# Kernel optimization log

Hardware: AMD Instinct MI355X
Metric: run time of the kernel (lower is better)

Reference implementation:

```python
import jax, jax.numpy as jnp
import numpy as np

B = 4096      # number of boards
H = 256       # n_hidden
SCALE = 0.0625  # 1/sqrt(H)
N_POLICY = 1858


def setup_inputs() -> dict:
    key = jax.random.key(0)
    ks = jax.random.split(key, 10)
    w_s = 1.0 / 16.0  # keep activations well-scaled
    return {
        "x": jax.random.normal(ks[0], (B * 64, H), jnp.float32),
        "w1": jax.random.normal(ks[1], (H, H), jnp.float32) * w_s,
        "b1": jax.random.normal(ks[2], (H,), jnp.float32) * w_s,
        "w2": jax.random.normal(ks[3], (H, H), jnp.float32) * w_s,
        "b2": jax.random.normal(ks[4], (H,), jnp.float32) * w_s,
        "w3": jax.random.normal(ks[5], (H, H), jnp.float32) * w_s,
        "b3": jax.random.normal(ks[6], (H,), jnp.float32) * w_s,
        "w4": jax.random.normal(ks[7], (4, H), jnp.float32) * w_s,
        "gather_idx": jax.random.randint(ks[8], (N_POLICY,), 0, 4288, jnp.int32),
    }


def reference(x, w1, b1, w2, b2, w3, b3, w4, gather_idx):
    out = jax.nn.relu(x @ w1.T + b1)                      # (B*64, H)
    q = (out @ w2.T + b2).reshape(-1, 64, H)              # (B, 64, H)
    k = (out @ w3.T + b3).reshape(-1, 64, H)              # (B, 64, H)
    logits = jnp.einsum("bqh,bkh->bqk", q, k) * SCALE     # (B, 64, 64)

    # promotion offsets from 8th-rank keys
    promo_keys = k[:, 56:64, :]                           # (B, 8, H)
    offs = jnp.einsum("bsh,ph->bps", promo_keys, w4)      # (B, 4, 8)
    offs = offs[:, :3, :] + offs[:, 3:4, :]               # (B, 3, 8) q/r/b + knight base
    off24 = jnp.transpose(offs, (0, 2, 1)).reshape(-1, 1, 24)  # (B,1,24) piece-fastest

    # knight promotion move logits: rank7 -> rank8 block
    n_promo = logits[:, 48:56, 56:64].reshape(-1, 64, 1)  # (B, 64, 1)
    n_promo = jnp.broadcast_to(n_promo, (n_promo.shape[0], 64, 3)).reshape(-1, 8, 24)

    promo = (off24 + n_promo).reshape(-1, 3, 64)          # (B, 3, 64)

    full = jnp.concatenate([logits, promo], axis=1).reshape(-1, 4288)  # (B, 4288)
    return jnp.take(full, gather_idx, axis=1)             # (B, 1858)
```

## Files before the change

kernel.cpp:

```cpp
#include <hip/hip_runtime.h>


typedef __bf16 bf16_t;
typedef __bf16 bf16x8 __attribute__((ext_vector_type(8)));
typedef float  f32x4  __attribute__((ext_vector_type(4)));

#define PSCALE 0.0625f
#define NPOL   1858
#define MFMA(a,b,c) __builtin_amdgcn_mfma_f32_16x16x32_bf16(a, b, c, 0, 0, 0)


__global__ void prep_w1(const float* __restrict__ w1, bf16_t* __restrict__ wfA) {
    int i = blockIdx.x * 256 + threadIdx.x;
    int j = i & 7, lane = (i >> 3) & 63, t = (i >> 9) & 7, n = (i >> 12) & 15;
    int row = n * 16 + (lane & 15);
    int col = t * 32 + (lane >> 4) * 8 + j;
    wfA[i] = (bf16_t)w1[row * 256 + col];
}

__global__ void prep_mat(const float* __restrict__ w2,
                         const float* __restrict__ w3,
                         bf16_t* __restrict__ wfM) {
    int m1 = blockIdx.x, m2 = threadIdx.x;
    float acc = 0.f;
    #pragma unroll 8
    for (int h = 0; h < 256; ++h)
        acc += w2[h * 256 + m1] * w3[h * 256 + m2];
    int t = m1 >> 5, quad = (m1 >> 3) & 3, j = m1 & 7;
    int n = m2 >> 4, l15 = m2 & 15;
    wfM[(((n * 8 + t) * 64) + (quad * 16 + l15)) * 8 + j] = (bf16_t)acc;
}

__global__ void prep_vecs(const float* __restrict__ w2,
                          const float* __restrict__ w3,
                          const float* __restrict__ b2,
                          const float* __restrict__ b3,
                          const float* __restrict__ w4,
                          float* __restrict__ flt) {
    int m = threadIdx.x;
    float c2 = 0.f, vv = 0.f, p0 = 0.f, p1 = 0.f, p2 = 0.f, p3 = 0.f;
    for (int h = 0; h < 256; ++h) {
        float w3h = w3[h * 256 + m];
        c2 += b2[h] * w3h;
        p0 += w4[h] * w3h;
        p1 += w4[256 + h] * w3h;
        p2 += w4[512 + h] * w3h;
        p3 += w4[768 + h] * w3h;
        vv += w2[h * 256 + m] * b3[h];
    }
    flt[m]        = c2;
    flt[256 + m]  = vv;
    flt[512 + m]  = p0;
    flt[768 + m]  = p1;
    flt[1024 + m] = p2;
    flt[1280 + m] = p3;
    if (m < 4) {
        float pb = 0.f;
        for (int h = 0; h < 256; ++h) pb += w4[m * 256 + h] * b3[h];
        flt[1536 + m] = pb;
    }
    if (m == 0) {
        float s = 0.f;
        for (int h = 0; h < 256; ++h) s += b2[h] * b3[h];
        flt[1540] = s;
    }
}


template <bool USE_WS>
__device__ __forceinline__ bf16x8 wfrag(const bf16_t* __restrict__ wl,
                                        const float* __restrict__ w,
                                        int n, int t, int lane) {
    if constexpr (USE_WS) {
        return *(const bf16x8*)(wl + (((n * 8 + t) * 64 + lane) << 3));
    } else {
        int l15 = lane & 15, quad = lane >> 4;
        const float* p = w + (n * 16 + l15) * 256 + t * 32 + quad * 8;
        f32x4 lo = *(const f32x4*)p;
        f32x4 hi = *(const f32x4*)(p + 4);
        bf16x8 v;
        v[0] = (bf16_t)lo[0]; v[1] = (bf16_t)lo[1];
        v[2] = (bf16_t)lo[2]; v[3] = (bf16_t)lo[3];
        v[4] = (bf16_t)hi[0]; v[5] = (bf16_t)hi[1];
        v[6] = (bf16_t)hi[2]; v[7] = (bf16_t)hi[3];
        return v;
    }
}

__device__ __forceinline__ int ks_off(int row, int col) {
    return ((row << 9) + (col << 1)) ^ ((row & 7) << 4);
}

__device__ __forceinline__ bf16x8 cvt8(const float* __restrict__ p) {
    f32x4 lo = *(const f32x4*)p;
    f32x4 hi = *(const f32x4*)(p + 4);
    bf16x8 v;
    v[0] = (bf16_t)lo[0]; v[1] = (bf16_t)lo[1];
    v[2] = (bf16_t)lo[2]; v[3] = (bf16_t)lo[3];
    v[4] = (bf16_t)hi[0]; v[5] = (bf16_t)hi[1];
    v[6] = (bf16_t)hi[2]; v[7] = (bf16_t)hi[3];
    return v;
}

__device__ __forceinline__ void mfma16(const bf16x8* inA, const bf16x8* inB,
                                       const bf16x8* w, f32x4& s0, f32x4& s1) {
    f32x4 a00 = {0.f,0.f,0.f,0.f}, a01 = {0.f,0.f,0.f,0.f};
    f32x4 a10 = {0.f,0.f,0.f,0.f}, a11 = {0.f,0.f,0.f,0.f};
    #pragma unroll
    for (int t = 0; t < 8; t += 2) {
        a00 = MFMA(inA[t],     w[t],     a00);
        a10 = MFMA(inB[t],     w[t],     a10);
        a01 = MFMA(inA[t + 1], w[t + 1], a01);
        a11 = MFMA(inB[t + 1], w[t + 1], a11);
    }
    s0 = a00 + a01;
    s1 = a10 + a11;
}

__device__ __forceinline__ void qtile_lds(const unsigned char* __restrict__ u_lds,
                                          const bf16x8* w, f32x4& s0, f32x4& s1,
                                          int quad, int l15, int R) {
    f32x4 a00 = {0.f,0.f,0.f,0.f}, a01 = {0.f,0.f,0.f,0.f};
    f32x4 a10 = {0.f,0.f,0.f,0.f}, a11 = {0.f,0.f,0.f,0.f};
    #pragma unroll
    for (int t = 0; t < 8; t += 2) {
        int oE = ks_off(R + l15, t * 32 + quad * 8);
        int oO = ks_off(R + l15, (t + 1) * 32 + quad * 8);
        bf16x8 xA0 = *(const bf16x8*)(u_lds + oE);
        bf16x8 xB0 = *(const bf16x8*)(u_lds + 32768 + oE);
        bf16x8 xA1 = *(const bf16x8*)(u_lds + oO);
        bf16x8 xB1 = *(const bf16x8*)(u_lds + 32768 + oO);
        a00 = MFMA(xA0, w[t],     a00);
        a10 = MFMA(xB0, w[t],     a10);
        a01 = MFMA(xA1, w[t + 1], a01);
        a11 = MFMA(xB1, w[t + 1], a11);
    }
    s0 = a00 + a01;
    s1 = a10 + a11;
}

template <bool RELU>
__device__ __forceinline__ void tile_store2(unsigned char* __restrict__ u_lds,
                                            const f32x4& sA, const f32x4& sB,
                                            float bv, int n,
                                            int quad, int l15, int R) {
    #pragma unroll
    for (int r2 = 0; r2 < 4; ++r2) {
        int off = ks_off(R + quad * 4 + r2, n * 16 + l15);
        float vA = sA[r2] + bv, vB = sB[r2] + bv;
        if (RELU) { vA = fmaxf(vA, 0.f); vB = fmaxf(vB, 0.f); }
        *(bf16_t*)(u_lds + off)         = (bf16_t)vA;
        *(bf16_t*)(u_lds + 32768 + off) = (bf16_t)vB;
    }
}

template <bool USE_WS, bool RELU>
__device__ __forceinline__ void layer2b(const bf16x8* inA, const bf16x8* inB,
                                        const bf16_t* __restrict__ wl,
                                        const float* __restrict__ wraw,
                                        const float* __restrict__ bias,
                                        unsigned char* __restrict__ u_lds,
                                        int lane, int quad, int l15, int R) {
    bf16x8 wA[4], wB[4];
    #pragma unroll
    for (int t = 0; t < 4; ++t)
        wA[t] = wfrag<USE_WS>(wl, wraw, 0, t, lane);

    #pragma unroll
    for (int n = 0; n < 16; ++n) {
        #pragma unroll
        for (int t = 0; t < 4; ++t)
            wB[t] = wfrag<USE_WS>(wl, wraw, n, 4 + t, lane);

        f32x4 aA0 = {0.f,0.f,0.f,0.f}, aA1 = {0.f,0.f,0.f,0.f};
        f32x4 aB0 = {0.f,0.f,0.f,0.f}, aB1 = {0.f,0.f,0.f,0.f};
        aA0 = MFMA(inA[0], wA[0], aA0);  aB0 = MFMA(inB[0], wA[0], aB0);
        aA1 = MFMA(inA[1], wA[1], aA1);  aB1 = MFMA(inB[1], wA[1], aB1);
        aA0 = MFMA(inA[2], wA[2], aA0);  aB0 = MFMA(inB[2], wA[2], aB0);
        aA1 = MFMA(inA[3], wA[3], aA1);  aB1 = MFMA(inB[3], wA[3], aB1);

        if (n < 15) {
            #pragma unroll
            for (int t = 0; t < 4; ++t)
                wA[t] = wfrag<USE_WS>(wl, wraw, n + 1, t, lane);
        }

        aA0 = MFMA(inA[4], wB[0], aA0);  aB0 = MFMA(inB[4], wB[0], aB0);
        aA1 = MFMA(inA[5], wB[1], aA1);  aB1 = MFMA(inB[5], wB[1], aB1);
        aA0 = MFMA(inA[6], wB[2], aA0);  aB0 = MFMA(inB[6], wB[2], aB0);
        aA1 = MFMA(inA[7], wB[3], aA1);  aB1 = MFMA(inB[7], wB[3], aB1);

        tile_store2<RELU>(u_lds, aA0 + aA1, aB0 + aB1,
                          bias[n * 16 + l15], n, quad, l15, R);
    }
}

__global__ __launch_bounds__(256, 2)
void policy_fused(const float* __restrict__ x,
                  const bf16_t* __restrict__ wfA,
                  const bf16_t* __restrict__ wfM,
                  const float* __restrict__ flt,
                  const float* __restrict__ b1,
                  const int*   __restrict__ gidx,
                  float* __restrict__ out,
                  int nbat) {
    __shared__ __align__(16) unsigned char u_lds[2 * 32768];
    __shared__ __align__(16) bf16_t qscr[4][2][16 * 40];
    __shared__ float promoLDS[2][4][8];
    __shared__ float patchLDS[2][8][8];
    __shared__ float qbLDS[2][64];

    const int tid  = threadIdx.x;
    const int lane = tid & 63;
    const int wv   = tid >> 6;
    const int quad = lane >> 4;
    const int l15  = lane & 15;
    const int R    = wv * 16;

    const int bat0 = blockIdx.x * 2;
    const bool has1 = (bat0 + 1) < nbat;
    const int bat1 = has1 ? bat0 + 1 : bat0;

    bf16x8 xaA[8], xaB[8];
    {
        const float* xr0 = x + ((size_t)bat0 * 64 + R + l15) * 256;
        const float* xr1 = x + ((size_t)bat1 * 64 + R + l15) * 256;
        #pragma unroll
        for (int t = 0; t < 8; ++t) {
            xaA[t] = cvt8(xr0 + t * 32 + quad * 8);
            xaB[t] = cvt8(xr1 + t * 32 + quad * 8);
        }
    }

    layer2b<true, true>(xaA, xaB, wfA, nullptr, b1, u_lds, lane, quad, l15, R);

    {
        float qbA = flt[1540], qbB = qbA;
        const float* vvec = flt + 256;
        #pragma unroll
        for (int t = 0; t < 8; ++t) {
            int off = ks_off(R + l15, t * 32 + quad * 8);
            bf16x8 oA = *(const bf16x8*)(u_lds + off);
            bf16x8 oB = *(const bf16x8*)(u_lds + 32768 + off);
            f32x4 va = *(const f32x4*)(vvec + t * 32 + quad * 8);
            f32x4 vb = *(const f32x4*)(vvec + t * 32 + quad * 8 + 4);
            qbA += (float)oA[0]*va[0] + (float)oA[1]*va[1]
                 + (float)oA[2]*va[2] + (float)oA[3]*va[3]
                 + (float)oA[4]*vb[0] + (float)oA[5]*vb[1]
                 + (float)oA[6]*vb[2] + (float)oA[7]*vb[3];
            qbB += (float)oB[0]*va[0] + (float)oB[1]*va[1]
                 + (float)oB[2]*va[2] + (float)oB[3]*va[3]
                 + (float)oB[4]*vb[0] + (float)oB[5]*vb[1]
                 + (float)oB[6]*vb[2] + (float)oB[7]*vb[3];
        }
        qbA += __shfl_xor(qbA, 16);  qbA += __shfl_xor(qbA, 32);
        qbB += __shfl_xor(qbB, 16);  qbB += __shfl_xor(qbB, 32);
        if (lane < 16) {
            qbLDS[0][R + lane] = qbA;
            qbLDS[1][R + lane] = qbB;
        }
    }

    bf16x8 wc[8], wn[8];
    #pragma unroll
    for (int t = 0; t < 8; ++t)
        wc[t] = wfrag<true>(wfM, nullptr, 0, t, lane);

    __syncthreads();

    f32x4 laA[4], laB[4];
    #pragma unroll
    for (int n = 0; n < 4; ++n) {
        laA[n] = (f32x4){0.f,0.f,0.f,0.f};
        laB[n] = (f32x4){0.f,0.f,0.f,0.f};
    }
    {
        bf16_t* qsA = &qscr[wv][0][0];
        bf16_t* qsB = &qscr[wv][1][0];

        #pragma unroll
        for (int t8 = 0; t8 < 8; ++t8) {
            const int n0 = 2 * t8, n1 = n0 + 1;

            #pragma unroll
            for (int t = 0; t < 8; ++t)
                wn[t] = wfrag<true>(wfM, nullptr, n1, t, lane);
            {
                f32x4 sA, sB;
                qtile_lds(u_lds, wc, sA, sB, quad, l15, R);
                float bv = flt[n0 * 16 + l15];
                #pragma unroll
                for (int r2 = 0; r2 < 4; ++r2) {
                    int qo = (quad * 4 + r2) * 40 + l15;
                    qsA[qo] = (bf16_t)(sA[r2] + bv);
                    qsB[qo] = (bf16_t)(sB[r2] + bv);
                }
            }

            if (t8 < 7) {
                #pragma unroll
                for (int t = 0; t < 8; ++t)
                    wc[t] = wfrag<true>(wfM, nullptr, n0 + 2, t, lane);
            }
            {
                f32x4 sA, sB;
                qtile_lds(u_lds, wn, sA, sB, quad, l15, R);
                float bv = flt[n1 * 16 + l15];
                #pragma unroll
                for (int r2 = 0; r2 < 4; ++r2) {
                    int qo = (quad * 4 + r2) * 40 + 16 + l15;
                    qsA[qo] = (bf16_t)(sA[r2] + bv);
                    qsB[qo] = (bf16_t)(sB[r2] + bv);
                }
            }

            bf16x8 qaA = *(const bf16x8*)(qsA + l15 * 40 + quad * 8);
            bf16x8 qaB = *(const bf16x8*)(qsB + l15 * 40 + quad * 8);
            #pragma unroll
            for (int np = 0; np < 4; ++np) {
                int ko = ks_off(np * 16 + l15, t8 * 32 + quad * 8);
                bf16x8 kA = *(const bf16x8*)(u_lds + ko);
                bf16x8 kB = *(const bf16x8*)(u_lds + 32768 + ko);
                laA[np] = MFMA(qaA, kA, laA[np]);
                laB[np] = MFMA(qaB, kB, laB[np]);
            }
        }
    }

    float qbra[4], qbrb[4];
    #pragma unroll
    for (int r2 = 0; r2 < 4; ++r2) {
        qbra[r2] = qbLDS[0][R + quad * 4 + r2];
        qbrb[r2] = qbLDS[1][R + quad * 4 + r2];
    }

    {
        int s = lane >> 3, seg = lane & 7;
        const float* wrow = flt + 512 + wv * 256;
        #pragma unroll
        for (int b = 0; b < 2; ++b) {
            const unsigned char* kb = u_lds + b * 32768;
            float p = 0.f;
            #pragma unroll
            for (int m = 0; m < 4; ++m) {
                bf16x8 kv = *(const bf16x8*)(kb + ks_off(56 + s, seg * 32 + m * 8));
                f32x4 wa = *(const f32x4*)(wrow + seg * 32 + m * 8);
                f32x4 wb = *(const f32x4*)(wrow + seg * 32 + m * 8 + 4);
                p += (float)kv[0] * wa[0] + (float)kv[1] * wa[1]
                   + (float)kv[2] * wa[2] + (float)kv[3] * wa[3]
                   + (float)kv[4] * wb[0] + (float)kv[5] * wb[1]
                   + (float)kv[6] * wb[2] + (float)kv[7] * wb[3];
            }
            p += __shfl_down(p, 4);
            p += __shfl_down(p, 2);
            p += __shfl_down(p, 1);
            if (seg == 0) promoLDS[b][wv][s] = p + flt[1536 + wv];
        }
    }

    if (wv == 3 && quad < 2 && l15 >= 8) {
        #pragma unroll
        for (int r2 = 0; r2 < 4; ++r2) {
            patchLDS[0][quad * 4 + r2][l15 - 8] = (laA[3][r2] + qbra[r2]) * PSCALE;
            patchLDS[1][quad * 4 + r2][l15 - 8] = (laB[3][r2] + qbrb[r2]) * PSCALE;
        }
    }

    __syncthreads();

    float* fb0 = (float*)u_lds;
    float* fb1 = (float*)(u_lds + 32768);
    #pragma unroll
    for (int n = 0; n < 4; ++n) {
        #pragma unroll
        for (int r2 = 0; r2 < 4; ++r2) {
            int idx = (R + quad * 4 + r2) * 64 + n * 16 + l15;
            fb0[idx] = (laA[n][r2] + qbra[r2]) * PSCALE;
            fb1[idx] = (laB[n][r2] + qbrb[r2]) * PSCALE;
        }
    }

    if (tid < 192) {
        int u = tid >> 6, vv2 = tid & 63;
        int mm = u * 64 + vv2;
        int r_ = mm / 24, c_ = mm - r_ * 24;
        int c3 = c_ / 3, cp = c_ - c3 * 3;
        fb0[(64 + u) * 64 + vv2] =
            promoLDS[0][cp][c3] + promoLDS[0][3][c3] + patchLDS[0][r_][c3];
        fb1[(64 + u) * 64 + vv2] =
            promoLDS[1][cp][c3] + promoLDS[1][3][c3] + patchLDS[1][r_][c3];
    }

    __syncthreads();

    {
        float* orow0 = out + (size_t)bat0 * NPOL;
        float* orow1 = out + (size_t)(bat0 + 1) * NPOL;
        int   idxv[8];
        float v0[8], v1[8];
        #pragma unroll
        for (int i = 0; i < 8; ++i) {
            int g = tid + i * 256;
            idxv[i] = (g < NPOL) ? gidx[g] : 0;
        }
        #pragma unroll
        for (int i = 0; i < 8; ++i) {
            v0[i] = fb0[idxv[i]];
            v1[i] = fb1[idxv[i]];
        }
        #pragma unroll
        for (int i = 0; i < 8; ++i) {
            int g = tid + i * 256;
            if (g < NPOL) {
                orow0[g] = v0[i];
                if (has1) orow1[g] = v1[i];
            }
        }
    }
}

__global__ __launch_bounds__(256, 2)
void policy_main(const float* __restrict__ x,
                 const float* __restrict__ w1,
                 const float* __restrict__ w2,
                 const float* __restrict__ w3,
                 const float* __restrict__ b1,
                 const float* __restrict__ b2,
                 const float* __restrict__ b3,
                 const float* __restrict__ w4,
                 const int*   __restrict__ gidx,
                 float* __restrict__ out,
                 int nbat) {
    __shared__ __align__(16) unsigned char u_lds[2 * 32768];
    __shared__ __align__(16) bf16_t qscr[4][2][16 * 40];
    __shared__ float promoLDS[2][4][8];
    __shared__ float patchLDS[2][8][8];

    const int tid  = threadIdx.x;
    const int lane = tid & 63;
    const int wv   = tid >> 6;
    const int quad = lane >> 4;
    const int l15  = lane & 15;
    const int R    = wv * 16;

    const int bat0 = blockIdx.x * 2;
    const bool has1 = (bat0 + 1) < nbat;
    const int bat1 = has1 ? bat0 + 1 : bat0;

    bf16x8 xaA[8], xaB[8];
    {
        const float* xr0 = x + ((size_t)bat0 * 64 + R + l15) * 256;
        const float* xr1 = x + ((size_t)bat1 * 64 + R + l15) * 256;
        #pragma unroll
        for (int t = 0; t < 8; ++t) {
            xaA[t] = cvt8(xr0 + t * 32 + quad * 8);
            xaB[t] = cvt8(xr1 + t * 32 + quad * 8);
        }
    }

    layer2b<false, true>(xaA, xaB, nullptr, w1, b1, u_lds, lane, quad, l15, R);
    bf16x8 oaA[8], oaB[8];
    #pragma unroll
    for (int t = 0; t < 8; ++t) {
        int off = ks_off(R + l15, t * 32 + quad * 8);
        oaA[t] = *(const bf16x8*)(u_lds + off);
        oaB[t] = *(const bf16x8*)(u_lds + 32768 + off);
    }

    layer2b<false, false>(oaA, oaB, nullptr, w3, b3, u_lds, lane, quad, l15, R);

    __syncthreads();

    f32x4 laA[4], laB[4];
    #pragma unroll
    for (int n = 0; n < 4; ++n) {
        laA[n] = (f32x4){0.f,0.f,0.f,0.f};
        laB[n] = (f32x4){0.f,0.f,0.f,0.f};
    }
    {
        bf16_t* qsA = &qscr[wv][0][0];
        bf16_t* qsB = &qscr[wv][1][0];
        bf16x8 wA[4], wB[4];
        #pragma unroll
        for (int t = 0; t < 4; ++t)
            wA[t] = wfrag<false>(nullptr, w2, 0, t, lane);

        #pragma unroll
        for (int t8 = 0; t8 < 8; ++t8) {
            const int n0 = 2 * t8, n1 = n0 + 1;
            #pragma unroll
            for (int t = 0; t < 4; ++t)
                wB[t] = wfrag<false>(nullptr, w2, n0, 4 + t, lane);
            {
                f32x4 cA0 = {0.f,0.f,0.f,0.f}, cA1 = {0.f,0.f,0.f,0.f};
                f32x4 cB0 = {0.f,0.f,0.f,0.f}, cB1 = {0.f,0.f,0.f,0.f};
                cA0 = MFMA(oaA[0], wA[0], cA0);  cB0 = MFMA(oaB[0], wA[0], cB0);
                cA1 = MFMA(oaA[1], wA[1], cA1);  cB1 = MFMA(oaB[1], wA[1], cB1);
                cA0 = MFMA(oaA[2], wA[2], cA0);  cB0 = MFMA(oaB[2], wA[2], cB0);
                cA1 = MFMA(oaA[3], wA[3], cA1);  cB1 = MFMA(oaB[3], wA[3], cB1);
                #pragma unroll
                for (int t = 0; t < 4; ++t)
                    wA[t] = wfrag<false>(nullptr, w2, n1, t, lane);
                cA0 = MFMA(oaA[4], wB[0], cA0);  cB0 = MFMA(oaB[4], wB[0], cB0);
                cA1 = MFMA(oaA[5], wB[1], cA1);  cB1 = MFMA(oaB[5], wB[1], cB1);
                cA0 = MFMA(oaA[6], wB[2], cA0);  cB0 = MFMA(oaB[6], wB[2], cB0);
                cA1 = MFMA(oaA[7], wB[3], cA1);  cB1 = MFMA(oaB[7], wB[3], cB1);
                f32x4 sA = cA0 + cA1, sB = cB0 + cB1;
                float bv = b2[n0 * 16 + l15];
                #pragma unroll
                for (int r2 = 0; r2 < 4; ++r2) {
                    int qo = (quad * 4 + r2) * 40 + l15;
                    qsA[qo] = (bf16_t)(sA[r2] + bv);
                    qsB[qo] = (bf16_t)(sB[r2] + bv);
                }
            }
            #pragma unroll
            for (int t = 0; t < 4; ++t)
                wB[t] = wfrag<false>(nullptr, w2, n1, 4 + t, lane);
            {
                f32x4 cA0 = {0.f,0.f,0.f,0.f}, cA1 = {0.f,0.f,0.f,0.f};
                f32x4 cB0 = {0.f,0.f,0.f,0.f}, cB1 = {0.f,0.f,0.f,0.f};
                cA0 = MFMA(oaA[0], wA[0], cA0);  cB0 = MFMA(oaB[0], wA[0], cB0);
                cA1 = MFMA(oaA[1], wA[1], cA1);  cB1 = MFMA(oaB[1], wA[1], cB1);
                cA0 = MFMA(oaA[2], wA[2], cA0);  cB0 = MFMA(oaB[2], wA[2], cB0);
                cA1 = MFMA(oaA[3], wA[3], cA1);  cB1 = MFMA(oaB[3], wA[3], cB1);
                if (t8 < 7) {
                    #pragma unroll
                    for (int t = 0; t < 4; ++t)
                        wA[t] = wfrag<false>(nullptr, w2, n0 + 2, t, lane);
                }
                cA0 = MFMA(oaA[4], wB[0], cA0);  cB0 = MFMA(oaB[4], wB[0], cB0);
                cA1 = MFMA(oaA[5], wB[1], cA1);  cB1 = MFMA(oaB[5], wB[1], cB1);
                cA0 = MFMA(oaA[6], wB[2], cA0);  cB0 = MFMA(oaB[6], wB[2], cB0);
                cA1 = MFMA(oaA[7], wB[3], cA1);  cB1 = MFMA(oaB[7], wB[3], cB1);
                f32x4 sA = cA0 + cA1, sB = cB0 + cB1;
                float bv = b2[n1 * 16 + l15];
                #pragma unroll
                for (int r2 = 0; r2 < 4; ++r2) {
                    int qo = (quad * 4 + r2) * 40 + 16 + l15;
                    qsA[qo] = (bf16_t)(sA[r2] + bv);
                    qsB[qo] = (bf16_t)(sB[r2] + bv);
                }
            }
            bf16x8 qaA = *(const bf16x8*)(qsA + l15 * 40 + quad * 8);
            bf16x8 qaB = *(const bf16x8*)(qsB + l15 * 40 + quad * 8);
            #pragma unroll
            for (int np = 0; np < 4; ++np) {
                int ko = ks_off(np * 16 + l15, t8 * 32 + quad * 8);
                bf16x8 kA = *(const bf16x8*)(u_lds + ko);
                bf16x8 kB = *(const bf16x8*)(u_lds + 32768 + ko);
                laA[np] = MFMA(qaA, kA, laA[np]);
                laB[np] = MFMA(qaB, kB, laB[np]);
            }
        }
    }

    {
        int s = lane >> 3, seg = lane & 7;
        const float* wrow = w4 + wv * 256;
        #pragma unroll
        for (int b = 0; b < 2; ++b) {
            const unsigned char* kb = u_lds + b * 32768;
            float p = 0.f;
            #pragma unroll
            for (int m = 0; m < 4; ++m) {
                bf16x8 kv = *(const bf16x8*)(kb + ks_off(56 + s, seg * 32 + m * 8));
                f32x4 wa = *(const f32x4*)(wrow + seg * 32 + m * 8);
                f32x4 wb = *(const f32x4*)(wrow + seg * 32 + m * 8 + 4);
                p += (float)kv[0] * wa[0] + (float)kv[1] * wa[1]
                   + (float)kv[2] * wa[2] + (float)kv[3] * wa[3]
                   + (float)kv[4] * wb[0] + (float)kv[5] * wb[1]
                   + (float)kv[6] * wb[2] + (float)kv[7] * wb[3];
            }
            p += __shfl_down(p, 4);
            p += __shfl_down(p, 2);
            p += __shfl_down(p, 1);
            if (seg == 0) promoLDS[b][wv][s] = p;
        }
    }

    if (wv == 3 && quad < 2 && l15 >= 8) {
        #pragma unroll
        for (int r2 = 0; r2 < 4; ++r2) {
            patchLDS[0][quad * 4 + r2][l15 - 8] = laA[3][r2] * PSCALE;
            patchLDS[1][quad * 4 + r2][l15 - 8] = laB[3][r2] * PSCALE;
        }
    }

    __syncthreads();

    float* fb0 = (float*)u_lds;
    float* fb1 = (float*)(u_lds + 32768);
    #pragma unroll
    for (int n = 0; n < 4; ++n) {
        #pragma unroll
        for (int r2 = 0; r2 < 4; ++r2) {
            int idx = (R + quad * 4 + r2) * 64 + n * 16 + l15;
            fb0[idx] = laA[n][r2] * PSCALE;
            fb1[idx] = laB[n][r2] * PSCALE;
        }
    }

    if (tid < 192) {
        int u = tid >> 6, vv2 = tid & 63;
        int mm = u * 64 + vv2;
        int r_ = mm / 24, c_ = mm - r_ * 24;
        int c3 = c_ / 3, cp = c_ - c3 * 3;
        fb0[(64 + u) * 64 + vv2] =
            promoLDS[0][cp][c3] + promoLDS[0][3][c3] + patchLDS[0][r_][c3];
        fb1[(64 + u) * 64 + vv2] =
            promoLDS[1][cp][c3] + promoLDS[1][3][c3] + patchLDS[1][r_][c3];
    }

    __syncthreads();

    {
        float* orow0 = out + (size_t)bat0 * NPOL;
        float* orow1 = out + (size_t)(bat0 + 1) * NPOL;
        int   idxv[8];
        float v0[8], v1[8];
        #pragma unroll
        for (int i = 0; i < 8; ++i) {
            int g = tid + i * 256;
            idxv[i] = (g < NPOL) ? gidx[g] : 0;
        }
        #pragma unroll
        for (int i = 0; i < 8; ++i) {
            v0[i] = fb0[idxv[i]];
            v1[i] = fb1[idxv[i]];
        }
        #pragma unroll
        for (int i = 0; i < 8; ++i) {
            int g = tid + i * 256;
            if (g < NPOL) {
                orow0[g] = v0[i];
                if (has1) orow1[g] = v1[i];
            }
        }
    }
}

extern "C" void kernel_launch(void* const* d_in, const int* in_sizes, int n_in,
                              void* d_out, int out_size, void* d_ws, size_t ws_size,
                              hipStream_t stream) {
    const float* x    = (const float*)d_in[0];
    const float* w1   = (const float*)d_in[1];
    const float* b1   = (const float*)d_in[2];
    const float* w2   = (const float*)d_in[3];
    const float* b2   = (const float*)d_in[4];
    const float* w3   = (const float*)d_in[5];
    const float* b3   = (const float*)d_in[6];
    const float* w4   = (const float*)d_in[7];
    const int*   gidx = (const int*)d_in[8];
    float* out = (float*)d_out;

    int nbat = in_sizes[0] / (64 * 256);
    int nblk = (nbat + 1) / 2;
    const size_t ws_needed = 262144 + 8192;

    if (ws_size >= ws_needed) {
        bf16_t* wfA = (bf16_t*)d_ws;
        bf16_t* wfM = wfA + 65536;
        float*  flt = (float*)((char*)d_ws + 262144);
        prep_w1  <<<256, 256, 0, stream>>>(w1, wfA);
        prep_mat <<<256, 256, 0, stream>>>(w2, w3, wfM);
        prep_vecs<<<1,   256, 0, stream>>>(w2, w3, b2, b3, w4, flt);
        policy_fused<<<nblk, 256, 0, stream>>>(
            x, wfA, wfM, flt, b1, gidx, out, nbat);
    } else {
        policy_main<<<nblk, 256, 0, stream>>>(
            x, w1, w2, w3, b1, b2, b3, w4, gidx, out, nbat);
    }
}
```

Measured before the change: 523.9 us.

## Split fused policy kernel across 8 waves with half-column layers

Replaces the 256-thread fused kernel with a 512-thread version. Each pair of waves now shares a 16-row group, and each wave computes half of the output columns of layer 1 and of the folded q·M layer. The q-projection is materialised in a second 64KB LDS buffer, so the per-tile q scratch and the fused q-tile/logit loop go away; logits are then computed per wave over its half of the key columns. The goal is more waves to hide MFMA and LDS latency and no redundant weight-fragment loads per wave. In exchange the block uses about 128KB of LDS, which may cap occupancy at one block per CU despite the launch bounds, and it adds barriers. The fallback kernel is also refactored to use shared helpers.

Result: slower. 536.1 us (+2.3%).

```diff
diff --git a/kernel.cpp b/kernel.cpp
--- a/kernel.cpp
+++ b/kernel.cpp
@@ -102,75 +102,24 @@
     return v;
 }
 
-__device__ __forceinline__ void mfma16(const bf16x8* inA, const bf16x8* inB,
-                                       const bf16x8* w, f32x4& s0, f32x4& s1) {
-    f32x4 a00 = {0.f,0.f,0.f,0.f}, a01 = {0.f,0.f,0.f,0.f};
-    f32x4 a10 = {0.f,0.f,0.f,0.f}, a11 = {0.f,0.f,0.f,0.f};
-    #pragma unroll
-    for (int t = 0; t < 8; t += 2) {
-        a00 = MFMA(inA[t],     w[t],     a00);
-        a10 = MFMA(inB[t],     w[t],     a10);
-        a01 = MFMA(inA[t + 1], w[t + 1], a01);
-        a11 = MFMA(inB[t + 1], w[t + 1], a11);
-    }
-    s0 = a00 + a01;
-    s1 = a10 + a11;
-}
-
-__device__ __forceinline__ void qtile_lds(const unsigned char* __restrict__ u_lds,
-                                          const bf16x8* w, f32x4& s0, f32x4& s1,
-                                          int quad, int l15, int R) {
-    f32x4 a00 = {0.f,0.f,0.f,0.f}, a01 = {0.f,0.f,0.f,0.f};
-    f32x4 a10 = {0.f,0.f,0.f,0.f}, a11 = {0.f,0.f,0.f,0.f};
-    #pragma unroll
-    for (int t = 0; t < 8; t += 2) {
-        int oE = ks_off(R + l15, t * 32 + quad * 8);
-        int oO = ks_off(R + l15, (t + 1) * 32 + quad * 8);
-        bf16x8 xA0 = *(const bf16x8*)(u_lds + oE);
-        bf16x8 xB0 = *(const bf16x8*)(u_lds + 32768 + oE);
-        bf16x8 xA1 = *(const bf16x8*)(u_lds + oO);
-        bf16x8 xB1 = *(const bf16x8*)(u_lds + 32768 + oO);
-        a00 = MFMA(xA0, w[t],     a00);
-        a10 = MFMA(xB0, w[t],     a10);
-        a01 = MFMA(xA1, w[t + 1], a01);
-        a11 = MFMA(xB1, w[t + 1], a11);
-    }
-    s0 = a00 + a01;
-    s1 = a10 + a11;
-}
-
 template <bool RELU>
-__device__ __forceinline__ void tile_store2(unsigned char* __restrict__ u_lds,
-                                            const f32x4& sA, const f32x4& sB,
-                                            float bv, int n,
+__device__ __forceinline__ void layer_half8(const bf16x8* inA, const bf16x8* inB,
+                                            const bf16_t* __restrict__ wl,
+                                            const float* __restrict__ bias,
+                                            unsigned char* __restrict__ dst,
+                                            int nb, int lane,
                                             int quad, int l15, int R) {
-    #pragma unroll
-    for (int r2 = 0; r2 < 4; ++r2) {
-        int off = ks_off(R + quad * 4 + r2, n * 16 + l15);
-        float vA = sA[r2] + bv, vB = sB[r2] + bv;
-        if (RELU) { vA = fmaxf(vA, 0.f); vB = fmaxf(vB, 0.f); }
-        *(bf16_t*)(u_lds + off)         = (bf16_t)vA;
-        *(bf16_t*)(u_lds + 32768 + off) = (bf16_t)vB;
-    }
-}
-
-template <bool USE_WS, bool RELU>
-__device__ __forceinline__ void layer2b(const bf16x8* inA, const bf16x8* inB,
-                                        const bf16_t* __restrict__ wl,
-                                        const float* __restrict__ wraw,
-                                        const float* __restrict__ bias,
-                                        unsigned char* __restrict__ u_lds,
-                                        int lane, int quad, int l15, int R) {
     bf16x8 wA[4], wB[4];
     #pragma unroll
     for (int t = 0; t < 4; ++t)
-        wA[t] = wfrag<USE_WS>(wl, wraw, 0, t, lane);
-
-    #pragma unroll
-    for (int n = 0; n < 16; ++n) {
+        wA[t] = wfrag<true>(wl, nullptr, nb, t, lane);
+
+    #pragma unroll
+    for (int k = 0; k < 8; ++k) {
+        const int n = nb + k;
         #pragma unroll
         for (int t = 0; t < 4; ++t)
-            wB[t] = wfrag<USE_WS>(wl, wraw, n, 4 + t, lane);
+            wB[t] = wfrag<true>(wl, nullptr, n, 4 + t, lane);
 
         f32x4 aA0 = {0.f,0.f,0.f,0.f}, aA1 = {0.f,0.f,0.f,0.f};
         f32x4 aB0 = {0.f,0.f,0.f,0.f}, aB1 = {0.f,0.f,0.f,0.f};
@@ -179,10 +128,10 @@
         aA0 = MFMA(inA[2], wA[2], aA0);  aB0 = MFMA(inB[2], wA[2], aB0);
         aA1 = MFMA(inA[3], wA[3], aA1);  aB1 = MFMA(inB[3], wA[3], aB1);
 
-        if (n < 15) {
+        if (k < 7) {
             #pragma unroll
             for (int t = 0; t < 4; ++t)
-                wA[t] = wfrag<USE_WS>(wl, wraw, n + 1, t, lane);
+                wA[t] = wfrag<true>(wl, nullptr, n + 1, t, lane);
         }
 
         aA0 = MFMA(inA[4], wB[0], aA0);  aB0 = MFMA(inB[4], wB[0], aB0);
@@ -190,22 +139,30 @@
         aA0 = MFMA(inA[6], wB[2], aA0);  aB0 = MFMA(inB[6], wB[2], aB0);
         aA1 = MFMA(inA[7], wB[3], aA1);  aB1 = MFMA(inB[7], wB[3], aB1);
 
-        tile_store2<RELU>(u_lds, aA0 + aA1, aB0 + aB1,
-                          bias[n * 16 + l15], n, quad, l15, R);
-    }
-}
-
-__global__ __launch_bounds__(256, 2)
-void policy_fused(const float* __restrict__ x,
-                  const bf16_t* __restrict__ wfA,
-                  const bf16_t* __restrict__ wfM,
-                  const float* __restrict__ flt,
-                  const float* __restrict__ b1,
-                  const int*   __restrict__ gidx,
-                  float* __restrict__ out,
-                  int nbat) {
-    __shared__ __align__(16) unsigned char u_lds[2 * 32768];
-    __shared__ __align__(16) bf16_t qscr[4][2][16 * 40];
+        f32x4 sA = aA0 + aA1, sB = aB0 + aB1;
+        float bv = bias[n * 16 + l15];
+        #pragma unroll
+        for (int r2 = 0; r2 < 4; ++r2) {
+            int off = ks_off(R + quad * 4 + r2, n * 16 + l15);
+            float vA = sA[r2] + bv, vB = sB[r2] + bv;
+            if (RELU) { vA = fmaxf(vA, 0.f); vB = fmaxf(vB, 0.f); }
+            *(bf16_t*)(dst + off)         = (bf16_t)vA;
+            *(bf16_t*)(dst + 32768 + off) = (bf16_t)vB;
+        }
+    }
+}
+
+__global__ __launch_bounds__(512, 2)
+void policy_fused8(const float* __restrict__ x,
+                   const bf16_t* __restrict__ wfA,
+                   const bf16_t* __restrict__ wfM,
+                   const float* __restrict__ flt,
+                   const float* __restrict__ b1,
+                   const int*   __restrict__ gidx,
+                   float* __restrict__ out,
+                   int nbat) {
+    __shared__ __align__(16) unsigned char u_lds[65536];
+    __shared__ __align__(16) unsigned char q2b[65536];
     __shared__ float promoLDS[2][4][8];
     __shared__ float patchLDS[2][8][8];
     __shared__ float qbLDS[2][64];
@@ -213,9 +170,12 @@
     const int tid  = threadIdx.x;
     const int lane = tid & 63;
     const int wv   = tid >> 6;
+    const int rg   = wv >> 1;
+    const int ch   = wv & 1;
     const int quad = lane >> 4;
     const int l15  = lane & 15;
-    const int R    = wv * 16;
+    const int R    = rg * 16;
+    const int NB   = ch * 8;
 
     const int bat0 = blockIdx.x * 2;
     const bool has1 = (bat0 + 1) < nbat;
@@ -232,137 +192,92 @@
         }
     }
 
-    layer2b<true, true>(xaA, xaB, wfA, nullptr, b1, u_lds, lane, quad, l15, R);
-
-    {
-        float qbA = flt[1540], qbB = qbA;
+    layer_half8<true>(xaA, xaB, wfA, b1, u_lds, NB, lane, quad, l15, R);
+
+    __syncthreads();
+
+    bf16x8 oaA[8], oaB[8];
+    #pragma unroll
+    for (int t = 0; t < 8; ++t) {
+        int off = ks_off(R + l15, t * 32 + quad * 8);
+        oaA[t] = *(const bf16x8*)(u_lds + off);
+        oaB[t] = *(const bf16x8*)(u_lds + 32768 + off);
+    }
+
+    layer_half8<false>(oaA, oaB, wfM, flt, q2b, NB, lane, quad, l15, R);
+
+    {
+        const bf16x8* oc = ch ? oaB : oaA;
+        float qb = flt[1540];
         const float* vvec = flt + 256;
         #pragma unroll
         for (int t = 0; t < 8; ++t) {
-            int off = ks_off(R + l15, t * 32 + quad * 8);
-            bf16x8 oA = *(const bf16x8*)(u_lds + off);
-            bf16x8 oB = *(const bf16x8*)(u_lds + 32768 + off);
             f32x4 va = *(const f32x4*)(vvec + t * 32 + quad * 8);
             f32x4 vb = *(const f32x4*)(vvec + t * 32 + quad * 8 + 4);
-            qbA += (float)oA[0]*va[0] + (float)oA[1]*va[1]
-                 + (float)oA[2]*va[2] + (float)oA[3]*va[3]
-                 + (float)oA[4]*vb[0] + (float)oA[5]*vb[1]
-                 + (float)oA[6]*vb[2] + (float)oA[7]*vb[3];
-            qbB += (float)oB[0]*va[0] + (float)oB[1]*va[1]
-                 + (float)oB[2]*va[2] + (float)oB[3]*va[3]
-                 + (float)oB[4]*vb[0] + (float)oB[5]*vb[1]
-                 + (float)oB[6]*vb[2] + (float)oB[7]*vb[3];
-        }
-        qbA += __shfl_xor(qbA, 16);  qbA += __shfl_xor(qbA, 32);
-        qbB += __shfl_xor(qbB, 16);  qbB += __shfl_xor(qbB, 32);
-        if (lane < 16) {
-            qbLDS[0][R + lane] = qbA;
-            qbLDS[1][R + lane] = qbB;
-        }
-    }
-
-    bf16x8 wc[8], wn[8];
-    #pragma unroll
-    for (int t = 0; t < 8; ++t)
-        wc[t] = wfrag<true>(wfM, nullptr, 0, t, lane);
+            qb += (float)oc[t][0]*va[0] + (float)oc[t][1]*va[1]
+                + (float)oc[t][2]*va[2] + (float)oc[t][3]*va[3]
+                + (float)oc[t][4]*vb[0] + (float)oc[t][5]*vb[1]
+                + (float)oc[t][6]*vb[2] + (float)oc[t][7]*vb[3];
+        }
+        qb += __shfl_xor(qb, 16);
+        qb += __shfl_xor(qb, 32);
+        if (lane < 16) qbLDS[ch][R + lane] = qb;
+    }
 
     __syncthreads();
 
-    f32x4 laA[4], laB[4];
-    #pragma unroll
-    for (int n = 0; n < 4; ++n) {
-        laA[n] = (f32x4){0.f,0.f,0.f,0.f};
-        laB[n] = (f32x4){0.f,0.f,0.f,0.f};
-    }
-    {
-        bf16_t* qsA = &qscr[wv][0][0];
-        bf16_t* qsB = &qscr[wv][1][0];
-
-        #pragma unroll
-        for (int t8 = 0; t8 < 8; ++t8) {
-            const int n0 = 2 * t8, n1 = n0 + 1;
-
-            #pragma unroll
-            for (int t = 0; t < 8; ++t)
-                wn[t] = wfrag<true>(wfM, nullptr, n1, t, lane);
-            {
-                f32x4 sA, sB;
-                qtile_lds(u_lds, wc, sA, sB, quad, l15, R);
-                float bv = flt[n0 * 16 + l15];
-                #pragma unroll
-                for (int r2 = 0; r2 < 4; ++r2) {
-                    int qo = (quad * 4 + r2) * 40 + l15;
-                    qsA[qo] = (bf16_t)(sA[r2] + bv);
-                    qsB[qo] = (bf16_t)(sB[r2] + bv);
-                }
-            }
-
-            if (t8 < 7) {
-                #pragma unroll
-                for (int t = 0; t < 8; ++t)
-                    wc[t] = wfrag<true>(wfM, nullptr, n0 + 2, t, lane);
-            }
-            {
-                f32x4 sA, sB;
-                qtile_lds(u_lds, wn, sA, sB, quad, l15, R);
-                float bv = flt[n1 * 16 + l15];
-                #pragma unroll
-                for (int r2 = 0; r2 < 4; ++r2) {
-                    int qo = (quad * 4 + r2) * 40 + 16 + l15;
-                    qsA[qo] = (bf16_t)(sA[r2] + bv);
-                    qsB[qo] = (bf16_t)(sB[r2] + bv);
-                }
-            }
-
-            bf16x8 qaA = *(const bf16x8*)(qsA + l15 * 40 + quad * 8);
-            bf16x8 qaB = *(const bf16x8*)(qsB + l15 * 40 + quad * 8);
-            #pragma unroll
-            for (int np = 0; np < 4; ++np) {
-                int ko = ks_off(np * 16 + l15, t8 * 32 + quad * 8);
-                bf16x8 kA = *(const bf16x8*)(u_lds + ko);
-                bf16x8 kB = *(const bf16x8*)(u_lds + 32768 + ko);
-                laA[np] = MFMA(qaA, kA, laA[np]);
-                laB[np] = MFMA(qaB, kB, laB[np]);
-            }
-        }
-    }
-
-    float qbra[4], qbrb[4];
-    #pragma unroll
-    for (int r2 = 0; r2 < 4; ++r2) {
-        qbra[r2] = qbLDS[0][R + quad * 4 + r2];
-        qbrb[r2] = qbLDS[1][R + quad * 4 + r2];
+    bf16x8 qaA[8], qaB[8];
+    #pragma unroll
+    for (int t = 0; t < 8; ++t) {
+        int off = ks_off(R + l15, t * 32 + quad * 8);
+        qaA[t] = *(const bf16x8*)(q2b + off);
+        qaB[t] = *(const bf16x8*)(q2b + 32768 + off);
+    }
+
+    f32x4 laA[2], laB[2];
+    laA[0] = (f32x4){0.f,0.f,0.f,0.f}; laA[1] = (f32x4){0.f,0.f,0.f,0.f};
+    laB[0] = (f32x4){0.f,0.f,0.f,0.f}; laB[1] = (f32x4){0.f,0.f,0.f,0.f};
+    #pragma unroll
+    for (int t8 = 0; t8 < 8; ++t8) {
+        #pragma unroll
+        for (int npl = 0; npl < 2; ++npl) {
+            int ko = ks_off((2 * ch + npl) * 16 + l15, t8 * 32 + quad * 8);
+            bf16x8 kA = *(const bf16x8*)(u_lds + ko);
+            bf16x8 kB = *(const bf16x8*)(u_lds + 32768 + ko);
+            laA[npl] = MFMA(qaA[t8], kA, laA[npl]);
+            laB[npl] = MFMA(qaB[t8], kB, laB[npl]);
+        }
     }
 
     {
         int s = lane >> 3, seg = lane & 7;
-        const float* wrow = flt + 512 + wv * 256;
-        #pragma unroll
-        for (int b = 0; b < 2; ++b) {
-            const unsigned char* kb = u_lds + b * 32768;
-            float p = 0.f;
-            #pragma unroll
-            for (int m = 0; m < 4; ++m) {
-                bf16x8 kv = *(const bf16x8*)(kb + ks_off(56 + s, seg * 32 + m * 8));
-                f32x4 wa = *(const f32x4*)(wrow + seg * 32 + m * 8);
-                f32x4 wb = *(const f32x4*)(wrow + seg * 32 + m * 8 + 4);
-                p += (float)kv[0] * wa[0] + (float)kv[1] * wa[1]
-                   + (float)kv[2] * wa[2] + (float)kv[3] * wa[3]
-                   + (float)kv[4] * wb[0] + (float)kv[5] * wb[1]
-                   + (float)kv[6] * wb[2] + (float)kv[7] * wb[3];
-            }
-            p += __shfl_down(p, 4);
-            p += __shfl_down(p, 2);
-            p += __shfl_down(p, 1);
-            if (seg == 0) promoLDS[b][wv][s] = p + flt[1536 + wv];
-        }
-    }
-
-    if (wv == 3 && quad < 2 && l15 >= 8) {
+        const float* wrow = flt + 512 + rg * 256;
+        const unsigned char* kb = u_lds + ch * 32768;
+        float pacc = 0.f;
+        #pragma unroll
+        for (int m = 0; m < 4; ++m) {
+            bf16x8 kv = *(const bf16x8*)(kb + ks_off(56 + s, seg * 32 + m * 8));
+            f32x4 wa = *(const f32x4*)(wrow + seg * 32 + m * 8);
+            f32x4 wb = *(const f32x4*)(wrow + seg * 32 + m * 8 + 4);
+            pacc += (float)kv[0] * wa[0] + (float)kv[1] * wa[1]
+                  + (float)kv[2] * wa[2] + (float)kv[3] * wa[3]
+                  + (float)kv[4] * wb[0] + (float)kv[5] * wb[1]
+                  + (float)kv[6] * wb[2] + (float)kv[7] * wb[3];
+        }
+        pacc += __shfl_down(pacc, 4);
+        pacc += __shfl_down(pacc, 2);
+        pacc += __shfl_down(pacc, 1);
+        if (seg == 0) promoLDS[ch][rg][s] = pacc + flt[1536 + rg];
+    }
+
+    if (wv == 7 && quad < 2 && l15 >= 8) {
         #pragma unroll
         for (int r2 = 0; r2 < 4; ++r2) {
-            patchLDS[0][quad * 4 + r2][l15 - 8] = (laA[3][r2] + qbra[r2]) * PSCALE;
-            patchLDS[1][quad * 4 + r2][l15 - 8] = (laB[3][r2] + qbrb[r2]) * PSCALE;
+            int row = 48 + quad * 4 + r2;
+            patchLDS[0][quad * 4 + r2][l15 - 8] =
+                (laA[1][r2] + qbLDS[0][row]) * PSCALE;
+            patchLDS[1][quad * 4 + r2][l15 - 8] =
+                (laB[1][r2] + qbLDS[1][row]) * PSCALE;
         }
     }
 
@@ -370,25 +285,34 @@
 
     float* fb0 = (float*)u_lds;
     float* fb1 = (float*)(u_lds + 32768);
-    #pragma unroll
-    for (int n = 0; n < 4; ++n) {
+    {
+        float qb0[4], qb1[4];
         #pragma unroll
         for (int r2 = 0; r2 < 4; ++r2) {
-            int idx = (R + quad * 4 + r2) * 64 + n * 16 + l15;
-            fb0[idx] = (laA[n][r2] + qbra[r2]) * PSCALE;
-            fb1[idx] = (laB[n][r2] + qbrb[r2]) * PSCALE;
-        }
-    }
-
-    if (tid < 192) {
-        int u = tid >> 6, vv2 = tid & 63;
+            qb0[r2] = qbLDS[0][R + quad * 4 + r2];
+            qb1[r2] = qbLDS[1][R + quad * 4 + r2];
+        }
+        #pragma unroll
+        for (int npl = 0; npl < 2; ++npl) {
+            #pragma unroll
+            for (int r2 = 0; r2 < 4; ++r2) {
+                int idx = (R + quad * 4 + r2) * 64 + (2 * ch + npl) * 16 + l15;
+                fb0[idx] = (laA[npl][r2] + qb0[r2]) * PSCALE;
+                fb1[idx] = (laB[npl][r2] + qb1[r2]) * PSCALE;
+            }
+        }
+    }
+
+    if (tid < 384) {
+        int b  = tid / 192;
+        int m  = tid - b * 192;
+        int u  = m >> 6, vv2 = m & 63;
         int mm = u * 64 + vv2;
         int r_ = mm / 24, c_ = mm - r_ * 24;
         int c3 = c_ / 3, cp = c_ - c3 * 3;
-        fb0[(64 + u) * 64 + vv2] =
-            promoLDS[0][cp][c3] + promoLDS[0][3][c3] + patchLDS[0][r_][c3];
-        fb1[(64 + u) * 64 + vv2] =
-            promoLDS[1][cp][c3] + promoLDS[1][3][c3] + patchLDS[1][r_][c3];
+        float* fb = b ? fb1 : fb0;
+        fb[(64 + u) * 64 + vv2] =
+            promoLDS[b][cp][c3] + promoLDS[b][3][c3] + patchLDS[b][r_][c3];
     }
 
     __syncthreads();
@@ -396,25 +320,83 @@
     {
         float* orow0 = out + (size_t)bat0 * NPOL;
         float* orow1 = out + (size_t)(bat0 + 1) * NPOL;
-        int   idxv[8];
-        float v0[8], v1[8];
-        #pragma unroll
-        for (int i = 0; i < 8; ++i) {
-            int g = tid + i * 256;
+        int   idxv[4];
+        float v0[4], v1[4];
+        #pragma unroll
+        for (int i = 0; i < 4; ++i) {
+            int g = tid + i * 512;
             idxv[i] = (g < NPOL) ? gidx[g] : 0;
         }
         #pragma unroll
-        for (int i = 0; i < 8; ++i) {
+        for (int i = 0; i < 4; ++i) {
             v0[i] = fb0[idxv[i]];
             v1[i] = fb1[idxv[i]];
         }
         #pragma unroll
-        for (int i = 0; i < 8; ++i) {
-            int g = tid + i * 256;
+        for (int i = 0; i < 4; ++i) {
+            int g = tid + i * 512;
             if (g < NPOL) {
                 orow0[g] = v0[i];
                 if (has1) orow1[g] = v1[i];
             }
+        }
+    }
+}
+
+__device__ __forceinline__ void mfma16f(const bf16x8* inA, const bf16x8* inB,
+                                        const bf16x8* w, f32x4& s0, f32x4& s1) {
+    f32x4 a00 = {0.f,0.f,0.f,0.f}, a01 = {0.f,0.f,0.f,0.f};
+    f32x4 a10 = {0.f,0.f,0.f,0.f}, a11 = {0.f,0.f,0.f,0.f};
+    #pragma unroll
+    for (int t = 0; t < 8; t += 2) {
+        a00 = MFMA(inA[t],     w[t],     a00);
+        a10 = MFMA(inB[t],     w[t],     a10);
+        a01 = MFMA(inA[t + 1], w[t + 1], a01);
+        a11 = MFMA(inB[t + 1], w[t + 1], a11);
+    }
+    s0 = a00 + a01;
+    s1 = a10 + a11;
+}
+
+template <bool RELU>
+__device__ __forceinline__ void layer_raw(const bf16x8* inA, const bf16x8* inB,
+                                          const float* __restrict__ wraw,
+                                          const float* __restrict__ bias,
+                                          unsigned char* __restrict__ u_lds,
+                                          int lane, int quad, int l15, int R) {
+    bf16x8 wA[4], wB[4];
+    #pragma unroll
+    for (int t = 0; t < 4; ++t)
+        wA[t] = wfrag<false>(nullptr, wraw, 0, t, lane);
+    #pragma unroll
+    for (int n = 0; n < 16; ++n) {
+        #pragma unroll
+        for (int t = 0; t < 4; ++t)
+            wB[t] = wfrag<false>(nullptr, wraw, n, 4 + t, lane);
+        f32x4 aA0 = {0.f,0.f,0.f,0.f}, aA1 = {0.f,0.f,0.f,0.f};
+        f32x4 aB0 = {0.f,0.f,0.f,0.f}, aB1 = {0.f,0.f,0.f,0.f};
+        aA0 = MFMA(inA[0], wA[0], aA0);  aB0 = MFMA(inB[0], wA[0], aB0);
+        aA1 = MFMA(inA[1], wA[1], aA1);  aB1 = MFMA(inB[1], wA[1], aB1);
+        aA0 = MFMA(inA[2], wA[2], aA0);  aB0 = MFMA(inB[2], wA[2], aB0);
+        aA1 = MFMA(inA[3], wA[3], aA1);  aB1 = MFMA(inB[3], wA[3], aB1);
+        if (n < 15) {
+            #pragma unroll
+            for (int t = 0; t < 4; ++t)
+                wA[t] = wfrag<false>(nullptr, wraw, n + 1, t, lane);
+        }
+        aA0 = MFMA(inA[4], wB[0], aA0);  aB0 = MFMA(inB[4], wB[0], aB0);
+        aA1 = MFMA(inA[5], wB[1], aA1);  aB1 = MFMA(inB[5], wB[1], aB1);
+        aA0 = MFMA(inA[6], wB[2], aA0);  aB0 = MFMA(inB[6], wB[2], aB0);
+        aA1 = MFMA(inA[7], wB[3], aA1);  aB1 = MFMA(inB[7], wB[3], aB1);
+        f32x4 sA = aA0 + aA1, sB = aB0 + aB1;
+        float bv = bias[n * 16 + l15];
+        #pragma unroll
+        for (int r2 = 0; r2 < 4; ++r2) {
+            int off = ks_off(R + quad * 4 + r2, n * 16 + l15);
+            float vA = sA[r2] + bv, vB = sB[r2] + bv;
+            if (RELU) { vA = fmaxf(vA, 0.f); vB = fmaxf(vB, 0.f); }
+            *(bf16_t*)(u_lds + off)         = (bf16_t)vA;
+            *(bf16_t*)(u_lds + 32768 + off) = (bf16_t)vB;
         }
     }
 }
@@ -458,7 +440,7 @@
         }
     }
 
-    layer2b<false, true>(xaA, xaB, nullptr, w1, b1, u_lds, lane, quad, l15, R);
+    layer_raw<true>(xaA, xaB, w1, b1, u_lds, lane, quad, l15, R);
     bf16x8 oaA[8], oaB[8];
     #pragma unroll
     for (int t = 0; t < 8; ++t) {
@@ -467,7 +449,7 @@
         oaB[t] = *(const bf16x8*)(u_lds + 32768 + off);
     }
 
-    layer2b<false, false>(oaA, oaB, nullptr, w3, b3, u_lds, lane, quad, l15, R);
+    layer_raw<false>(oaA, oaB, w3, b3, u_lds, lane, quad, l15, R);
 
     __syncthreads();
 
@@ -492,20 +474,10 @@
             for (int t = 0; t < 4; ++t)
                 wB[t] = wfrag<false>(nullptr, w2, n0, 4 + t, lane);
             {
-                f32x4 cA0 = {0.f,0.f,0.f,0.f}, cA1 = {0.f,0.f,0.f,0.f};
-                f32x4 cB0 = {0.f,0.f,0.f,0.f}, cB1 = {0.f,0.f,0.f,0.f};
-                cA0 = MFMA(oaA[0], wA[0], cA0);  cB0 = MFMA(oaB[0], wA[0], cB0);
-                cA1 = MFMA(oaA[1], wA[1], cA1);  cB1 = MFMA(oaB[1], wA[1], cB1);
-                cA0 = MFMA(oaA[2], wA[2], cA0);  cB0 = MFMA(oaB[2], wA[2], cB0);
-                cA1 = MFMA(oaA[3], wA[3], cA1);  cB1 = MFMA(oaB[3], wA[3], cB1);
-                #pragma unroll
-                for (int t = 0; t < 4; ++t)
-                    wA[t] = wfrag<false>(nullptr, w2, n1, t, lane);
-                cA0 = MFMA(oaA[4], wB[0], cA0);  cB0 = MFMA(oaB[4], wB[0], cB0);
-                cA1 = MFMA(oaA[5], wB[1], cA1);  cB1 = MFMA(oaB[5], wB[1], cB1);
-                cA0 = MFMA(oaA[6], wB[2], cA0);  cB0 = MFMA(oaB[6], wB[2], cB0);
-                cA1 = MFMA(oaA[7], wB[3], cA1);  cB1 = MFMA(oaB[7], wB[3], cB1);
-                f32x4 sA = cA0 + cA1, sB = cB0 + cB1;
+                f32x4 sA, sB;
+                bf16x8 wfull[8] = {wA[0], wA[1], wA[2], wA[3],
+                                   wB[0], wB[1], wB[2], wB[3]};
+                mfma16f(oaA, oaB, wfull, sA, sB);
                 float bv = b2[n0 * 16 + l15];
                 #pragma unroll
                 for (int r2 = 0; r2 < 4; ++r2) {
@@ -516,24 +488,15 @@
             }
             #pragma unroll
             for (int t = 0; t < 4; ++t)
+                wA[t] = wfrag<false>(nullptr, w2, n1, t, lane);
+            #pragma unroll
+            for (int t = 0; t < 4; ++t)
                 wB[t] = wfrag<false>(nullptr, w2, n1, 4 + t, lane);
             {
-                f32x4 cA0 = {0.f,0.f,0.f,0.f}, cA1 = {0.f,0.f,0.f,0.f};
-                f32x4 cB0 = {0.f,0.f,0.f,0.f}, cB1 = {0.f,0.f,0.f,0.f};
-                cA0 = MFMA(oaA[0], wA[0], cA0);  cB0 = MFMA(oaB[0], wA[0], cB0);
-                cA1 = MFMA(oaA[1], wA[1], cA1);  cB1 = MFMA(oaB[1], wA[1], cB1);
-                cA0 = MFMA(oaA[2], wA[2], cA0);  cB0 = MFMA(oaB[2], wA[2], cB0);
-                cA1 = MFMA(oaA[3], wA[3], cA1);  cB1 = MFMA(oaB[3], wA[3], cB1);
-                if (t8 < 7) {
-                    #pragma unroll
-                    for (int t = 0; t < 4; ++t)
-                        wA[t] = wfrag<false>(nullptr, w2, n0 + 2, t, lane);
-                }
-                cA0 = MFMA(oaA[4], wB[0], cA0);  cB0 = MFMA(oaB[4], wB[0], cB0);
-                cA1 = MFMA(oaA[5], wB[1], cA1);  cB1 = MFMA(oaB[5], wB[1], cB1);
-                cA0 = MFMA(oaA[6], wB[2], cA0);  cB0 = MFMA(oaB[6], wB[2], cB0);
-                cA1 = MFMA(oaA[7], wB[3], cA1);  cB1 = MFMA(oaB[7], wB[3], cB1);
-                f32x4 sA = cA0 + cA1, sB = cB0 + cB1;
+                f32x4 sA, sB;
+                bf16x8 wfull[8] = {wA[0], wA[1], wA[2], wA[3],
+                                   wB[0], wB[1], wB[2], wB[3]};
+                mfma16f(oaA, oaB, wfull, sA, sB);
                 float bv = b2[n1 * 16 + l15];
                 #pragma unroll
                 for (int r2 = 0; r2 < 4; ++r2) {
@@ -541,6 +504,11 @@
                     qsA[qo] = (bf16_t)(sA[r2] + bv);
                     qsB[qo] = (bf16_t)(sB[r2] + bv);
                 }
+            }
+            if (t8 < 7) {
+                #pragma unroll
+                for (int t = 0; t < 4; ++t)
+                    wA[t] = wfrag<false>(nullptr, w2, n0 + 2, t, lane);
             }
             bf16x8 qaA = *(const bf16x8*)(qsA + l15 * 40 + quad * 8);
             bf16x8 qaB = *(const bf16x8*)(qsB + l15 * 40 + quad * 8);
@@ -665,7 +633,7 @@
         prep_w1  <<<256, 256, 0, stream>>>(w1, wfA);
         prep_mat <<<256, 256, 0, stream>>>(w2, w3, wfM);
         prep_vecs<<<1,   256, 0, stream>>>(w2, w3, b2, b3, w4, flt);
-        policy_fused<<<nblk, 256, 0, stream>>>(
+        policy_fused8<<<nblk, 512, 0, stream>>>(
             x, wfA, wfM, flt, b1, gidx, out, nbat);
     } else {
         policy_main<<<nblk, 256, 0, stream>>>(
```
